# Kernel optimization log

Hardware: AMD Instinct MI355X
Metric: run time of the kernel (lower is better)

## Reference

```python
import jax, jax.numpy as jnp
import numpy as np

EPS = 1e-5

def binarize(x):
    # sign with 0 -> -1
    return jnp.where(x <= 0, -1.0, 1.0).astype(x.dtype)

def conv2d(x, w, stride=1, padding=0, dilation=1):
    return jax.lax.conv_general_dilated(
        x, w, (stride, stride), [(padding, padding), (padding, padding)],
        rhs_dilation=(dilation, dilation),
        dimension_numbers=('NCHW', 'OIHW', 'NCHW'))

def bin_conv(x, w, stride=1, padding=0, dilation=1):
    return conv2d(binarize(x), binarize(w), stride, padding, dilation)

def bn(x, g, b, m, v):
    inv = g / jnp.sqrt(v + EPS)          # [C]
    return x * inv[None, :, None, None] + (b - m * inv)[None, :, None, None]

def prelu(x, a):
    return jnp.where(x >= 0, x, a * x)   # a is scalar (nn.PReLU default)

def setup_inputs() -> dict:
    key = jax.random.key(0)
    ks = jax.random.split(key, 16)
    B, C, H, W = 8, 128, 128, 256
    Ci = C // 4  # proj_ratio = 4
    def bn_params(k, c):
        k1, k2, k3, k4 = jax.random.split(k, 4)
        return (jax.random.uniform(k1, (c,), jnp.float32, 0.5, 1.5),
                jax.random.normal(k2, (c,), jnp.float32) * 0.1,
                jax.random.normal(k3, (c,), jnp.float32) * 0.1,
                jax.random.uniform(k4, (c,), jnp.float32, 0.5, 1.5))
    g1, b1, m1, v1 = bn_params(ks[1], Ci)
    g2, b2, m2, v2 = bn_params(ks[3], Ci)
    g3, b3, m3, v3 = bn_params(ks[5], C)
    return {
        'x': jax.random.normal(ks[0], (B, C, H, W), jnp.float32),
        'w1': jax.random.normal(ks[6], (Ci, C, 1, 1), jnp.float32) * 0.1,
        'g1': g1, 'b1': b1, 'm1': m1, 'v1': v1,
        'a1': jnp.float32(0.25),
        'w2': jax.random.normal(ks[7], (Ci, Ci, 3, 3), jnp.float32) * 0.1,
        'g2': g2, 'b2': b2, 'm2': m2, 'v2': v2,
        'a2': jnp.float32(0.25),
        'w3': jax.random.normal(ks[8], (C, Ci, 1, 1), jnp.float32) * 0.1,
        'g3': g3, 'b3': b3, 'm3': m3, 'v3': v3,
        'a3': jnp.float32(0.25),
        'a_out': jnp.float32(0.25),
    }

def reference(x, w1, g1, b1, m1, v1, a1,
              w2, g2, b2, m2, v2, a2,
              w3, g3, b3, m3, v3, a3, a_out):
    identity = x
    h = prelu(bn(bin_conv(x, w1), g1, b1, m1, v1), a1)          # 1x1 proj
    h = prelu(bn(bin_conv(h, w2, padding=1), g2, b2, m2, v2), a2)  # 3x3
    h = prelu(bn(bin_conv(h, w3), g3, b3, m3, v3), a3)          # 1x1 expand
    return prelu(h + identity, a_out)
```

## Files before the change

kernel.cpp:

```cpp
#include <hip/hip_runtime.h>
#include <stdint.h>
#include <math.h>


#define EPS 1e-5f
constexpr int B = 8, C = 128, Ci = 32, H = 128, W = 256;
constexpr int HW = H * W;
constexpr int P  = B * HW;

constexpr int WS_S1 = 1024;
constexpr int WS_S2 = 1024 + P;

__global__ __launch_bounds__(256) void prep_kernel(
    const float* __restrict__ w1,
    const float* __restrict__ g1, const float* __restrict__ b1,
    const float* __restrict__ m1, const float* __restrict__ v1,
    const float* __restrict__ w2,
    const float* __restrict__ g2, const float* __restrict__ b2,
    const float* __restrict__ m2, const float* __restrict__ v2,
    const float* __restrict__ w3,
    const float* __restrict__ g3, const float* __restrict__ b3,
    const float* __restrict__ m3, const float* __restrict__ v3,
    uint32_t* __restrict__ ws)
{
    int t = threadIdx.x;
    float* wsf = (float*)ws;

    if (t < 128) {
        int ci = t >> 2, wd = t & 3;
        const float* src = w1 + ci * C + wd * 32;
        uint32_t m = 0;
        #pragma unroll
        for (int j = 0; j < 32; ++j) m |= (src[j] > 0.f ? 1u : 0u) << j;
        ws[t] = m;
    }
    for (int idx = t; idx < 288; idx += 256) {
        int ci = idx / 9, tap = idx % 9;
        uint32_t m = 0;
        for (int cj = 0; cj < 32; ++cj)
            m |= (w2[(ci * Ci + cj) * 9 + tap] > 0.f ? 1u : 0u) << cj;
        ws[128 + idx] = m;
    }
    if (t < 128) {
        const float* src = w3 + t * Ci;
        uint32_t m = 0;
        #pragma unroll
        for (int j = 0; j < 32; ++j) m |= (src[j] > 0.f ? 1u : 0u) << j;
        ws[416 + t] = m;
    }
    if (t < 32) {
        float inv1 = g1[t] / sqrtf(v1[t] + EPS);
        wsf[544 + t] = m1[t] - b1[t] / inv1;
        float inv2 = g2[t] / sqrtf(v2[t] + EPS);
        wsf[576 + t] = m2[t] - b2[t] / inv2;
    }
    if (t < 128) {
        float i3 = g3[t] / sqrtf(v3[t] + EPS);
        wsf[608 + t] = i3;
        wsf[736 + t] = b3[t] - m3[t] * i3;
    }
}

__global__ __launch_bounds__(256) void k1_kernel(
    const float* __restrict__ x, const uint32_t* __restrict__ ws,
    uint32_t* __restrict__ s1)
{
    __shared__ uint32_t w1p[128];
    __shared__ float T1[32];
    int t = threadIdx.x;
    if (t < 128) w1p[t] = ws[t];
    if (t < 32)  T1[t] = ((const float*)ws)[544 + t];
    __syncthreads();

    int p   = blockIdx.x * 256 + t;
    int b   = p >> 15;
    int rem = p & (HW - 1);
    const float* xb = x + (size_t)b * C * HW + rem;

    uint32_t m[4];
    #pragma unroll
    for (int wd = 0; wd < 4; ++wd) {
        uint32_t mm = 0;
        #pragma unroll
        for (int j = 0; j < 32; ++j) {
            float v = xb[(size_t)(wd * 32 + j) * HW];
            mm |= (v > 0.f ? 1u : 0u) << j;
        }
        m[wd] = mm;
    }

    uint32_t out = 0;
    #pragma unroll
    for (int ci = 0; ci < 32; ++ci) {
        int neq = __popc(m[0] ^ w1p[ci * 4 + 0]) + __popc(m[1] ^ w1p[ci * 4 + 1])
                + __popc(m[2] ^ w1p[ci * 4 + 2]) + __popc(m[3] ^ w1p[ci * 4 + 3]);
        float y1 = (float)(128 - 2 * neq);
        out |= (y1 > T1[ci] ? 1u : 0u) << ci;
    }
    s1[p] = out;
}

__global__ __launch_bounds__(256) void k2_kernel(
    const uint32_t* __restrict__ s1, const uint32_t* __restrict__ ws,
    uint32_t* __restrict__ s2)
{
    __shared__ uint32_t w2p[288];
    __shared__ float T2[32];
    int t = threadIdx.x;
    for (int i = t; i < 288; i += 256) w2p[i] = ws[128 + i];
    if (t < 32) T2[t] = ((const float*)ws)[576 + t];
    __syncthreads();

    int p   = blockIdx.x * 256 + t;
    int b   = p >> 15;
    int rem = p & (HW - 1);
    int h   = rem >> 8;
    int w   = rem & 255;

    uint32_t n[9];
    uint32_t vmask = 0;
    int nv = 0;
    #pragma unroll
    for (int dy = -1; dy <= 1; ++dy) {
        #pragma unroll
        for (int dx = -1; dx <= 1; ++dx) {
            int tap = (dy + 1) * 3 + (dx + 1);
            int hh = h + dy, wv = w + dx;
            bool ok = (hh >= 0) & (hh < H) & (wv >= 0) & (wv < W);
            uint32_t val = 0;
            if (ok) val = s1[b * HW + hh * W + wv];
            n[tap] = val;
            vmask |= ok ? (1u << tap) : 0u;
            nv += ok ? 1 : 0;
        }
    }

    uint32_t out = 0;
    #pragma unroll
    for (int ci = 0; ci < 32; ++ci) {
        int neq = 0;
        #pragma unroll
        for (int tap = 0; tap < 9; ++tap) {
            int pc = __popc(n[tap] ^ w2p[ci * 9 + tap]);
            neq += ((vmask >> tap) & 1u) ? pc : 0;
        }
        float y2 = (float)(32 * nv - 2 * neq);
        out |= (y2 > T2[ci] ? 1u : 0u) << ci;
    }
    s2[p] = out;
}

__global__ __launch_bounds__(256) void k3_kernel(
    const float* __restrict__ x, const uint32_t* __restrict__ s2,
    const uint32_t* __restrict__ ws,
    const float* __restrict__ a3p, const float* __restrict__ aoutp,
    float* __restrict__ out)
{
    __shared__ uint32_t w3p[128];
    __shared__ float inv3[128], c3[128];
    int t = threadIdx.x;
    if (t < 128) {
        w3p[t]  = ws[416 + t];
        inv3[t] = ((const float*)ws)[608 + t];
        c3[t]   = ((const float*)ws)[736 + t];
    }
    __syncthreads();

    float a3 = a3p[0], aout = aoutp[0];
    int p   = blockIdx.x * 256 + t;
    int b   = p >> 15;
    int rem = p & (HW - 1);
    size_t base = (size_t)b * C * HW + rem;
    uint32_t sw = s2[p];

    #pragma unroll 8
    for (int c = 0; c < C; ++c) {
        int y3 = 32 - 2 * __popc(sw ^ w3p[c]);
        float hv = fmaf((float)y3, inv3[c], c3[c]);
        hv = hv < 0.f ? a3 * hv : hv;
        float o = hv + x[base + (size_t)c * HW];
        o = o < 0.f ? aout * o : o;
        out[base + (size_t)c * HW] = o;
    }
}

extern "C" void kernel_launch(void* const* d_in, const int* in_sizes, int n_in,
                              void* d_out, int out_size, void* d_ws, size_t ws_size,
                              hipStream_t stream)
{
    const float* x  = (const float*)d_in[0];
    const float* w1 = (const float*)d_in[1];
    const float* g1 = (const float*)d_in[2];
    const float* b1 = (const float*)d_in[3];
    const float* m1 = (const float*)d_in[4];
    const float* v1 = (const float*)d_in[5];
    const float* w2 = (const float*)d_in[7];
    const float* g2 = (const float*)d_in[8];
    const float* b2 = (const float*)d_in[9];
    const float* m2 = (const float*)d_in[10];
    const float* v2 = (const float*)d_in[11];
    const float* w3 = (const float*)d_in[13];
    const float* g3 = (const float*)d_in[14];
    const float* b3 = (const float*)d_in[15];
    const float* m3 = (const float*)d_in[16];
    const float* v3 = (const float*)d_in[17];
    const float* a3 = (const float*)d_in[18];
    const float* ao = (const float*)d_in[19];

    uint32_t* ws = (uint32_t*)d_ws;
    uint32_t* s1 = ws + WS_S1;
    uint32_t* s2 = ws + WS_S2;
    float* out = (float*)d_out;

    hipLaunchKernelGGL(prep_kernel, dim3(1), dim3(256), 0, stream,
                       w1, g1, b1, m1, v1, w2, g2, b2, m2, v2, w3, g3, b3, m3, v3, ws);
    hipLaunchKernelGGL(k1_kernel, dim3(P / 256), dim3(256), 0, stream, x, ws, s1);
    hipLaunchKernelGGL(k2_kernel, dim3(P / 256), dim3(256), 0, stream, s1, ws, s2);
    hipLaunchKernelGGL(k3_kernel, dim3(P / 256), dim3(256), 0, stream, x, s2, ws, a3, ao, out);
}
```

Measured before the change: 304.4 us.

## Process four pixels per thread in binarized 1x1 and 3x3 conv kernels

The first two stages now have each thread handle four adjacent pixels. In the 1x1 projection kernel, activations are read as float4 and four bitmasks are packed at once. In the 3x3 kernel, three rows of six s1 words are loaded per thread, so neighbouring pixels share loads and popcount weight reads from LDS. The goal is fewer load instructions, better vectorized memory access and more reuse, at the cost of a quarter of the threads and higher register pressure per thread.

```diff
diff --git a/kernel.cpp b/kernel.cpp
--- a/kernel.cpp
+++ b/kernel.cpp
@@ -6,6 +6,7 @@
 #define EPS 1e-5f
 constexpr int B = 8, C = 128, Ci = 32, H = 128, W = 256;
 constexpr int HW = H * W;
+constexpr int HW4 = HW / 4;
 constexpr int P  = B * HW;
 
 constexpr int WS_S1 = 1024;
@@ -62,8 +63,8 @@
 }
 
 __global__ __launch_bounds__(256) void k1_kernel(
-    const float* __restrict__ x, const uint32_t* __restrict__ ws,
-    uint32_t* __restrict__ s1)
+    const float4* __restrict__ x4, const uint32_t* __restrict__ ws,
+    uint4* __restrict__ s1v)
 {
     __shared__ uint32_t w1p[128];
     __shared__ float T1[32];
@@ -72,37 +73,44 @@
     if (t < 32)  T1[t] = ((const float*)ws)[544 + t];
     __syncthreads();
 
-    int p   = blockIdx.x * 256 + t;
-    int b   = p >> 15;
-    int rem = p & (HW - 1);
-    const float* xb = x + (size_t)b * C * HW + rem;
-
-    uint32_t m[4];
+    int g  = blockIdx.x * 256 + t;
+    int b  = g >> 13;
+    int r4 = g & (HW4 - 1);
+    const float4* xb = x4 + (size_t)b * C * HW4 + r4;
+
+    uint32_t m[4][4];
     #pragma unroll
     for (int wd = 0; wd < 4; ++wd) {
-        uint32_t mm = 0;
+        uint32_t a0 = 0, a1 = 0, a2 = 0, a3 = 0;
         #pragma unroll
         for (int j = 0; j < 32; ++j) {
-            float v = xb[(size_t)(wd * 32 + j) * HW];
-            mm |= (v > 0.f ? 1u : 0u) << j;
+            float4 v = xb[(size_t)(wd * 32 + j) * HW4];
+            a0 |= (v.x > 0.f ? 1u : 0u) << j;
+            a1 |= (v.y > 0.f ? 1u : 0u) << j;
+            a2 |= (v.z > 0.f ? 1u : 0u) << j;
+            a3 |= (v.w > 0.f ? 1u : 0u) << j;
         }
-        m[wd] = mm;
-    }
-
-    uint32_t out = 0;
+        m[0][wd] = a0; m[1][wd] = a1; m[2][wd] = a2; m[3][wd] = a3;
+    }
+
+    uint32_t o[4] = {0, 0, 0, 0};
     #pragma unroll
     for (int ci = 0; ci < 32; ++ci) {
-        int neq = __popc(m[0] ^ w1p[ci * 4 + 0]) + __popc(m[1] ^ w1p[ci * 4 + 1])
-                + __popc(m[2] ^ w1p[ci * 4 + 2]) + __popc(m[3] ^ w1p[ci * 4 + 3]);
-        float y1 = (float)(128 - 2 * neq);
-        out |= (y1 > T1[ci] ? 1u : 0u) << ci;
-    }
-    s1[p] = out;
+        uint32_t q0 = w1p[ci*4], q1 = w1p[ci*4+1], q2 = w1p[ci*4+2], q3 = w1p[ci*4+3];
+        float T = T1[ci];
+        #pragma unroll
+        for (int k = 0; k < 4; ++k) {
+            int neq = __popc(m[k][0]^q0) + __popc(m[k][1]^q1)
+                    + __popc(m[k][2]^q2) + __popc(m[k][3]^q3);
+            o[k] |= ((float)(128 - 2*neq) > T ? 1u : 0u) << ci;
+        }
+    }
+    s1v[g] = make_uint4(o[0], o[1], o[2], o[3]);
 }
 
 __global__ __launch_bounds__(256) void k2_kernel(
     const uint32_t* __restrict__ s1, const uint32_t* __restrict__ ws,
-    uint32_t* __restrict__ s2)
+    uint4* __restrict__ s2v)
 {
     __shared__ uint32_t w2p[288];
     __shared__ float T2[32];
@@ -111,43 +119,60 @@
     if (t < 32) T2[t] = ((const float*)ws)[576 + t];
     __syncthreads();
 
-    int p   = blockIdx.x * 256 + t;
-    int b   = p >> 15;
-    int rem = p & (HW - 1);
+    int g   = blockIdx.x * 256 + t;
+    int p0  = g << 2;
+    int b   = p0 >> 15;
+    int rem = p0 & (HW - 1);
     int h   = rem >> 8;
     int w   = rem & 255;
 
-    uint32_t n[9];
-    uint32_t vmask = 0;
-    int nv = 0;
-    #pragma unroll
-    for (int dy = -1; dy <= 1; ++dy) {
-        #pragma unroll
-        for (int dx = -1; dx <= 1; ++dx) {
-            int tap = (dy + 1) * 3 + (dx + 1);
-            int hh = h + dy, wv = w + dx;
-            bool ok = (hh >= 0) & (hh < H) & (wv >= 0) & (wv < W);
-            uint32_t val = 0;
-            if (ok) val = s1[b * HW + hh * W + wv];
-            n[tap] = val;
-            vmask |= ok ? (1u << tap) : 0u;
-            nv += ok ? 1 : 0;
+    bool leftok = (w > 0), rightok = (w < 252);
+    uint32_t arr[3][6];
+    bool rowok[3];
+    #pragma unroll
+    for (int r = 0; r < 3; ++r) {
+        int hh = h + r - 1;
+        bool ok = (hh >= 0) && (hh < H);
+        rowok[r] = ok;
+        int idx = b * HW + hh * W + w;
+        uint4 mid = make_uint4(0u, 0u, 0u, 0u);
+        if (ok) mid = *(const uint4*)(s1 + idx);
+        arr[r][1] = mid.x; arr[r][2] = mid.y; arr[r][3] = mid.z; arr[r][4] = mid.w;
+        arr[r][0] = (ok && leftok)  ? s1[idx - 1] : 0u;
+        arr[r][5] = (ok && rightok) ? s1[idx + 4] : 0u;
+    }
+    bool wok[6] = {leftok, true, true, true, true, rightok};
+
+    uint32_t o[4];
+    #pragma unroll
+    for (int i = 0; i < 4; ++i) {
+        bool tv[9];
+        int nv = 0;
+        #pragma unroll
+        for (int r = 0; r < 3; ++r)
+            #pragma unroll
+            for (int dxi = 0; dxi < 3; ++dxi) {
+                bool v = rowok[r] && wok[i + dxi];
+                tv[r*3 + dxi] = v;
+                nv += v ? 1 : 0;
+            }
+        float base2 = (float)(32 * nv);
+        uint32_t ob = 0;
+        #pragma unroll
+        for (int ci = 0; ci < 32; ++ci) {
+            int neq = 0;
+            #pragma unroll
+            for (int r = 0; r < 3; ++r)
+                #pragma unroll
+                for (int dxi = 0; dxi < 3; ++dxi) {
+                    int pc = __popc(arr[r][i + dxi] ^ w2p[ci*9 + r*3 + dxi]);
+                    neq += tv[r*3 + dxi] ? pc : 0;
+                }
+            ob |= ((base2 - (float)(2*neq)) > T2[ci] ? 1u : 0u) << ci;
         }
-    }
-
-    uint32_t out = 0;
-    #pragma unroll
-    for (int ci = 0; ci < 32; ++ci) {
-        int neq = 0;
-        #pragma unroll
-        for (int tap = 0; tap < 9; ++tap) {
-            int pc = __popc(n[tap] ^ w2p[ci * 9 + tap]);
-            neq += ((vmask >> tap) & 1u) ? pc : 0;
-        }
-        float y2 = (float)(32 * nv - 2 * neq);
-        out |= (y2 > T2[ci] ? 1u : 0u) << ci;
-    }
-    s2[p] = out;
+        o[i] = ob;
+    }
+    s2v[g] = make_uint4(o[0], o[1], o[2], o[3]);
 }
 
 __global__ __launch_bounds__(256) void k3_kernel(
@@ -210,11 +235,13 @@
     uint32_t* ws = (uint32_t*)d_ws;
     uint32_t* s1 = ws + WS_S1;
     uint32_t* s2 = ws + WS_S2;
-    float* out = (float*)d_out;
 
     hipLaunchKernelGGL(prep_kernel, dim3(1), dim3(256), 0, stream,
                        w1, g1, b1, m1, v1, w2, g2, b2, m2, v2, w3, g3, b3, m3, v3, ws);
-    hipLaunchKernelGGL(k1_kernel, dim3(P / 256), dim3(256), 0, stream, x, ws, s1);
-    hipLaunchKernelGGL(k2_kernel, dim3(P / 256), dim3(256), 0, stream, s1, ws, s2);
-    hipLaunchKernelGGL(k3_kernel, dim3(P / 256), dim3(256), 0, stream, x, s2, ws, a3, ao, out);
-}
+    hipLaunchKernelGGL(k1_kernel, dim3(P / 1024), dim3(256), 0, stream,
+                       (const float4*)x, ws, (uint4*)s1);
+    hipLaunchKernelGGL(k2_kernel, dim3(P / 1024), dim3(256), 0, stream,
+                       s1, ws, (uint4*)s2);
+    hipLaunchKernelGGL(k3_kernel, dim3(P / 256), dim3(256), 0, stream,
+                       x, s2, ws, a3, ao, (float*)d_out);
+}
```

Result: slower. 311.1 us (+2.2%).
